# Kernel tuning notes

Hardware: AMD Instinct MI355X
Metric: run time of the kernel (lower is better)

## Reference

```python
import jax, jax.numpy as jnp
import numpy as np

N_NODES = 50000
N_EDGES = 800000
ND = 64   # node_dim
HD = 128  # hidden_dim
ED = 32   # edge_dim


def setup_inputs() -> dict:
    key = jax.random.key(0)
    ks = jax.random.split(key, 16)
    init = lambda k, shape: (jax.random.normal(k, shape, jnp.float32)
                             / np.float32(np.sqrt(shape[0])))
    h = jax.random.normal(ks[0], (N_NODES, ND), jnp.float32)
    x = jax.random.normal(ks[1], (N_NODES, 3), jnp.float32) * 10.0
    edge_index = jax.random.randint(ks[2], (2, N_EDGES), 0, N_NODES, dtype=jnp.int64)
    # realistic edge distances = actual pairwise distances of sampled edges
    edge_dist = jnp.linalg.norm(x[edge_index[0]] - x[edge_index[1]], axis=-1)
    in_dim = 2 * ND + ED
    return {
        "h": h, "x": x, "edge_index": edge_index, "edge_dist": edge_dist,
        # edge_mlp: Linear(1, ED) -> SiLU -> Linear(ED, ED)
        "We1": init(ks[3], (1, ED)), "be1": jnp.zeros((ED,), jnp.float32),
        "We2": init(ks[4], (ED, ED)), "be2": jnp.zeros((ED,), jnp.float32),
        # node_mlp: Linear(in_dim, HD) -> SiLU -> Linear(HD, ND)
        "Wn1": init(ks[5], (in_dim, HD)), "bn1": jnp.zeros((HD,), jnp.float32),
        "Wn2": init(ks[6], (HD, ND)), "bn2": jnp.zeros((ND,), jnp.float32),
        # coord_mlp: Linear(in_dim, HD) -> SiLU -> Linear(HD, 1, bias=False)
        "Wc1": init(ks[7], (in_dim, HD)), "bc1": jnp.zeros((HD,), jnp.float32),
        "Wc2": init(ks[8], (HD, 1)),
    }


def reference(h, x, edge_index, edge_dist,
              We1, be1, We2, be2,
              Wn1, bn1, Wn2, bn2,
              Wc1, bc1, Wc2):
    n = h.shape[0]
    src, dst = edge_index[0], edge_index[1]
    # edge_mlp on scalar distance -> [E, ED]
    e = jax.nn.silu(edge_dist[:, None] @ We1 + be1) @ We2 + be2
    # gather + concat -> [E, 2*ND + ED]
    m_input = jnp.concatenate([h[src], h[dst], e], axis=-1)
    # node messages [E, ND]
    m = jax.nn.silu(m_input @ Wn1 + bn1) @ Wn2 + bn2
    h_agg = jax.ops.segment_sum(m, dst, num_segments=n)
    # coord update weight [E, 1]
    coord_weight = jax.nn.silu(m_input @ Wc1 + bc1) @ Wc2
    dir_vec = x[src] - x[dst]
    dir_len = jnp.clip(jnp.linalg.norm(dir_vec, axis=-1, keepdims=True), 1e-8)
    coord_update = coord_weight * (dir_vec / dir_len)
    x_agg = jax.ops.segment_sum(coord_update, dst, num_segments=n)
    return h + h_agg, x + x_agg
```

## Files before the change

kernel.cpp:

```cpp
#include <hip/hip_runtime.h>


#define NN 50000
#define NE 800000
#define NDIM 64
#define HDIM 128
#define EDIM 32
#define NTILES (NE / 64)
#define MSTRIDE 168
#define HSTRIDE 136
#define NH (NN * NDIM)
#define NX (NN * 3)

typedef __bf16 bf16x8 __attribute__((ext_vector_type(8)));
typedef float f32x4 __attribute__((ext_vector_type(4)));
typedef unsigned short ushort8 __attribute__((ext_vector_type(8)));
typedef unsigned short ushort4v __attribute__((ext_vector_type(4)));

__device__ __forceinline__ unsigned short f2bf(float f) {
    union { float f; unsigned int u; } c; c.f = f;
    unsigned int r = c.u + 0x7fffu + ((c.u >> 16) & 1u);
    return (unsigned short)(r >> 16);
}
__device__ __forceinline__ float bf2f(unsigned short u) {
    union { unsigned int u; float f; } c; c.u = ((unsigned int)u) << 16;
    return c.f;
}
__device__ __forceinline__ float silu(float v) { return v / (1.0f + __expf(-v)); }

__device__ __forceinline__ bf16x8 ld_frag(const unsigned short* p) {
    union { ushort8 u; bf16x8 v; } c;
    c.u = *(const ushort8*)p;
    return c.v;
}
__device__ __forceinline__ bf16x8 mk_frag(const unsigned short* u) {
    union { ushort8 uu; bf16x8 v; } c;
#pragma unroll
    for (int j = 0; j < 8; ++j) c.uu[j] = u[j];
    return c.v;
}

__global__ void init_out(const float* __restrict__ h, const float* __restrict__ x,
                         float* __restrict__ out) {
    int i = blockIdx.x * 256 + threadIdx.x;
    if (i < NH) out[i] = h[i];
    else if (i < NH + NX) out[i] = x[i - NH];
}

__global__ __launch_bounds__(256, 2) void egnn_edges(
    const float* __restrict__ h, const float* __restrict__ x,
    const int* __restrict__ srcg, const int* __restrict__ dstg,
    const float* __restrict__ dist,
    const float* __restrict__ We1, const float* __restrict__ be1,
    const float* __restrict__ We2, const float* __restrict__ be2,
    const float* __restrict__ Wn1, const float* __restrict__ bn1,
    const float* __restrict__ Wn2, const float* __restrict__ bn2,
    const float* __restrict__ Wc1, const float* __restrict__ bc1,
    const float* __restrict__ Wc2,
    float* __restrict__ outh, float* __restrict__ outx) {

    __shared__ __align__(16) unsigned short mlds[64 * MSTRIDE];
    __shared__ __align__(16) unsigned short hl[64 * HSTRIDE];
    __shared__ int src_l[64];
    __shared__ int dst_l[64];
    __shared__ float dist_l[64];
    __shared__ float we1_l[32], be1_l[32], be2_l[32];
    __shared__ float we2_l[32 * 32];
    __shared__ float wc2_l[128];
    __shared__ float part_l[256];

    const int tid  = threadIdx.x;
    const int w    = tid >> 6;
    const int lane = tid & 63;
    const int l15  = lane & 15;
    const int quad = lane >> 4;

    if (tid < 32) { we1_l[tid] = We1[tid]; be1_l[tid] = be1[tid]; be2_l[tid] = be2[tid]; }
    if (tid < 128) wc2_l[tid] = Wc2[tid];
    for (int i = tid; i < 1024; i += 256) we2_l[i] = We2[i];

    bf16x8 wn1f[5][2], wc1f[5][2];
#pragma unroll
    for (int kc = 0; kc < 5; ++kc) {
#pragma unroll
        for (int nt = 0; nt < 2; ++nt) {
            unsigned short un[8], uc[8];
            const int n = w * 32 + nt * 16 + l15;
#pragma unroll
            for (int j = 0; j < 8; ++j) {
                const int k = kc * 32 + quad * 8 + j;
                un[j] = f2bf(Wn1[k * HDIM + n]);
                uc[j] = f2bf(Wc1[k * HDIM + n]);
            }
            wn1f[kc][nt] = mk_frag(un);
            wc1f[kc][nt] = mk_frag(uc);
        }
    }
    bf16x8 wn2f[4];
#pragma unroll
    for (int kc = 0; kc < 4; ++kc) {
        unsigned short u[8];
        const int n = w * 16 + l15;
#pragma unroll
        for (int j = 0; j < 8; ++j) {
            const int k = kc * 32 + quad * 8 + j;
            u[j] = f2bf(Wn2[k * NDIM + n]);
        }
        wn2f[kc] = mk_frag(u);
    }
    const float biasN0 = bn1[w * 32 + l15];
    const float biasN1 = bn1[w * 32 + 16 + l15];
    const float biasC0 = bc1[w * 32 + l15];
    const float biasC1 = bc1[w * 32 + 16 + l15];
    const float bias2v = bn2[w * 16 + l15];

    for (int tile = blockIdx.x; tile < NTILES; tile += gridDim.x) {
        __syncthreads();

        if (tid < 64) {
            const int e = tile * 64 + tid;
            src_l[tid] = srcg[e];
            dst_l[tid] = dstg[e];
            dist_l[tid] = dist[e];
        }
        __syncthreads();

        {
            const int c4 = tid & 15, sub = tid >> 4;
#pragma unroll
            for (int it = 0; it < 4; ++it) {
                const int el = sub + it * 16;
                const float4 hs = *(const float4*)(h + (size_t)src_l[el] * NDIM + c4 * 4);
                const float4 hd = *(const float4*)(h + (size_t)dst_l[el] * NDIM + c4 * 4);
                ushort4v us = { f2bf(hs.x), f2bf(hs.y), f2bf(hs.z), f2bf(hs.w) };
                ushort4v ud = { f2bf(hd.x), f2bf(hd.y), f2bf(hd.z), f2bf(hd.w) };
                *(ushort4v*)&mlds[el * MSTRIDE + c4 * 4] = us;
                *(ushort4v*)&mlds[el * MSTRIDE + 64 + c4 * 4] = ud;
            }
        }
        {
            const int el = tid >> 2, part = tid & 3;
            const float dv = dist_l[el];
            float o[8];
#pragma unroll
            for (int j = 0; j < 8; ++j) o[j] = be2_l[part * 8 + j];
#pragma unroll
            for (int k = 0; k < 32; ++k) {
                const float sk = silu(dv * we1_l[k] + be1_l[k]);
#pragma unroll
                for (int j = 0; j < 8; ++j) o[j] += sk * we2_l[k * 32 + part * 8 + j];
            }
            ushort4v a = { f2bf(o[0]), f2bf(o[1]), f2bf(o[2]), f2bf(o[3]) };
            ushort4v b = { f2bf(o[4]), f2bf(o[5]), f2bf(o[6]), f2bf(o[7]) };
            *(ushort4v*)&mlds[el * MSTRIDE + 128 + part * 8] = a;
            *(ushort4v*)&mlds[el * MSTRIDE + 128 + part * 8 + 4] = b;
        }
        __syncthreads();

        f32x4 accN[4][2], accC[4][2];
#pragma unroll
        for (int mt = 0; mt < 4; ++mt) {
            accN[mt][0] = (f32x4){biasN0, biasN0, biasN0, biasN0};
            accN[mt][1] = (f32x4){biasN1, biasN1, biasN1, biasN1};
            accC[mt][0] = (f32x4){biasC0, biasC0, biasC0, biasC0};
            accC[mt][1] = (f32x4){biasC1, biasC1, biasC1, biasC1};
        }
#pragma unroll
        for (int kc = 0; kc < 5; ++kc) {
            bf16x8 af[4];
#pragma unroll
            for (int mt = 0; mt < 4; ++mt)
                af[mt] = ld_frag(&mlds[(mt * 16 + l15) * MSTRIDE + kc * 32 + quad * 8]);
#pragma unroll
            for (int mt = 0; mt < 4; ++mt) {
#pragma unroll
                for (int nt = 0; nt < 2; ++nt) {
                    accN[mt][nt] = __builtin_amdgcn_mfma_f32_16x16x32_bf16(
                        af[mt], wn1f[kc][nt], accN[mt][nt], 0, 0, 0);
                    accC[mt][nt] = __builtin_amdgcn_mfma_f32_16x16x32_bf16(
                        af[mt], wc1f[kc][nt], accC[mt][nt], 0, 0, 0);
                }
            }
        }

#pragma unroll
        for (int mt = 0; mt < 4; ++mt)
#pragma unroll
            for (int nt = 0; nt < 2; ++nt)
#pragma unroll
                for (int r = 0; r < 4; ++r)
                    hl[(mt * 16 + quad * 4 + r) * HSTRIDE + w * 32 + nt * 16 + l15] =
                        f2bf(silu(accN[mt][nt][r]));
        __syncthreads();

        f32x4 acc2[4];
#pragma unroll
        for (int mt = 0; mt < 4; ++mt) acc2[mt] = (f32x4){bias2v, bias2v, bias2v, bias2v};
#pragma unroll
        for (int kc = 0; kc < 4; ++kc) {
#pragma unroll
            for (int mt = 0; mt < 4; ++mt) {
                bf16x8 a2 = ld_frag(&hl[(mt * 16 + l15) * HSTRIDE + kc * 32 + quad * 8]);
                acc2[mt] = __builtin_amdgcn_mfma_f32_16x16x32_bf16(a2, wn2f[kc], acc2[mt], 0, 0, 0);
            }
        }
#pragma unroll
        for (int mt = 0; mt < 4; ++mt) {
#pragma unroll
            for (int r = 0; r < 4; ++r) {
                const int el = mt * 16 + quad * 4 + r;
                atomicAdd(outh + (size_t)dst_l[el] * NDIM + w * 16 + l15, acc2[mt][r]);
            }
        }
        __syncthreads();

#pragma unroll
        for (int mt = 0; mt < 4; ++mt)
#pragma unroll
            for (int nt = 0; nt < 2; ++nt)
#pragma unroll
                for (int r = 0; r < 4; ++r)
                    hl[(mt * 16 + quad * 4 + r) * HSTRIDE + w * 32 + nt * 16 + l15] =
                        f2bf(silu(accC[mt][nt][r]));
        __syncthreads();

        {
            const int el = tid & 63, part = tid >> 6;
            float s = 0.0f;
#pragma unroll
            for (int k = 0; k < 32; ++k) {
                const int kk = part * 32 + k;
                s += bf2f(hl[el * HSTRIDE + kk]) * wc2_l[kk];
            }
            part_l[part * 64 + el] = s;
        }
        __syncthreads();

        if (tid < 64) {
            const float cw = part_l[tid] + part_l[64 + tid] + part_l[128 + tid] + part_l[192 + tid];
            const int sn = src_l[tid], dn = dst_l[tid];
            const float dx = x[sn * 3 + 0] - x[dn * 3 + 0];
            const float dy = x[sn * 3 + 1] - x[dn * 3 + 1];
            const float dz = x[sn * 3 + 2] - x[dn * 3 + 2];
            float len = sqrtf(dx * dx + dy * dy + dz * dz);
            len = fmaxf(len, 1e-8f);
            const float f = cw / len;
            atomicAdd(outx + (size_t)dn * 3 + 0, f * dx);
            atomicAdd(outx + (size_t)dn * 3 + 1, f * dy);
            atomicAdd(outx + (size_t)dn * 3 + 2, f * dz);
        }
    }
}

extern "C" void kernel_launch(void* const* d_in, const int* in_sizes, int n_in,
                              void* d_out, int out_size, void* d_ws, size_t ws_size,
                              hipStream_t stream) {
    const float* h    = (const float*)d_in[0];
    const float* x    = (const float*)d_in[1];
    const int*   ei   = (const int*)d_in[2];
    const float* dist = (const float*)d_in[3];
    const float* We1  = (const float*)d_in[4];
    const float* be1  = (const float*)d_in[5];
    const float* We2  = (const float*)d_in[6];
    const float* be2  = (const float*)d_in[7];
    const float* Wn1  = (const float*)d_in[8];
    const float* bn1  = (const float*)d_in[9];
    const float* Wn2  = (const float*)d_in[10];
    const float* bn2  = (const float*)d_in[11];
    const float* Wc1  = (const float*)d_in[12];
    const float* bc1  = (const float*)d_in[13];
    const float* Wc2  = (const float*)d_in[14];

    float* outh = (float*)d_out;
    float* outx = outh + (size_t)NH;

    init_out<<<(NH + NX + 255) / 256, 256, 0, stream>>>(h, x, (float*)d_out);
    egnn_edges<<<512, 256, 0, stream>>>(h, x, ei, ei + NE, dist,
                                        We1, be1, We2, be2,
                                        Wn1, bn1, Wn2, bn2,
                                        Wc1, bc1, Wc2,
                                        outh, outx);
}
```

Measured before the change: 418.4 us.

## Fold edge MLP second layer into first GEMM, prepack bf16 h, fuse coord reduction

Precomputes We2·Wn1/Wc1 (and bias folding) in a prep kernel so the per-edge edge-MLP only needs SiLU of the first layer, removing the 32x32 per-edge matmul. Converts h to bf16 once so gathers read half the bytes, permutes hidden columns so SiLU results store as packed pairs, and replaces the LDS round-trip for the coord weight with an in-register shuffle reduction. Raises occupancy target to 3 blocks/SM and doubles grid size. Adds extra prep launches and workspace use, and folding weights in bf16 changes rounding slightly.

```diff
diff --git a/kernel.cpp b/kernel.cpp
--- a/kernel.cpp
+++ b/kernel.cpp
@@ -5,13 +5,18 @@
 #define NE 800000
 #define NDIM 64
 #define HDIM 128
-#define EDIM 32
 #define NTILES (NE / 64)
 #define MSTRIDE 168
 #define HSTRIDE 136
 #define NH (NN * NDIM)
 #define NX (NN * 3)
 
+#define WS_HBF    0
+#define WS_WN1P   6400000
+#define WS_WC1P   6440960
+#define WS_BN1P   6481920
+#define WS_BC1P   6482432
+
 typedef __bf16 bf16x8 __attribute__((ext_vector_type(8)));
 typedef float f32x4 __attribute__((ext_vector_type(4)));
 typedef unsigned short ushort8 __attribute__((ext_vector_type(8)));
@@ -22,12 +27,12 @@
     unsigned int r = c.u + 0x7fffu + ((c.u >> 16) & 1u);
     return (unsigned short)(r >> 16);
 }
-__device__ __forceinline__ float bf2f(unsigned short u) {
-    union { unsigned int u; float f; } c; c.u = ((unsigned int)u) << 16;
-    return c.f;
-}
-__device__ __forceinline__ float silu(float v) { return v / (1.0f + __expf(-v)); }
-
+__device__ __forceinline__ unsigned int pk2bf(float a, float b) {
+    return (unsigned int)f2bf(a) | ((unsigned int)f2bf(b) << 16);
+}
+__device__ __forceinline__ float silu(float v) {
+    return v * __builtin_amdgcn_rcpf(1.0f + __expf(-v));
+}
 __device__ __forceinline__ bf16x8 ld_frag(const unsigned short* p) {
     union { ushort8 u; bf16x8 v; } c;
     c.u = *(const ushort8*)p;
@@ -47,15 +52,58 @@
     else if (i < NH + NX) out[i] = x[i - NH];
 }
 
-__global__ __launch_bounds__(256, 2) void egnn_edges(
-    const float* __restrict__ h, const float* __restrict__ x,
+__global__ void prep_h(const float* __restrict__ h, unsigned short* __restrict__ hbf) {
+    int i = (blockIdx.x * 256 + threadIdx.x) * 4;
+    if (i < NH) {
+        float4 v = *(const float4*)(h + i);
+        ushort4v u = { f2bf(v.x), f2bf(v.y), f2bf(v.z), f2bf(v.w) };
+        *(ushort4v*)(hbf + i) = u;
+    }
+}
+
+__global__ void prep_w(const float* __restrict__ We2, const float* __restrict__ be2,
+                       const float* __restrict__ Wn1, const float* __restrict__ bn1,
+                       const float* __restrict__ Wc1, const float* __restrict__ bc1,
+                       unsigned short* __restrict__ wn1p, unsigned short* __restrict__ wc1p,
+                       float* __restrict__ bn1p, float* __restrict__ bc1p) {
+    int idx = blockIdx.x * 256 + threadIdx.x;
+    if (idx >= 160 * 128) return;
+    int k = idx >> 7, n = idx & 127;
+    float vn, vc;
+    if (k < 128) {
+        vn = Wn1[k * HDIM + n];
+        vc = Wc1[k * HDIM + n];
+    } else {
+        int i = k - 128;
+        float sn = 0.0f, sc = 0.0f;
+        for (int j = 0; j < 32; ++j) {
+            float w = We2[i * 32 + j];
+            sn += w * Wn1[(128 + j) * HDIM + n];
+            sc += w * Wc1[(128 + j) * HDIM + n];
+        }
+        vn = sn; vc = sc;
+    }
+    wn1p[idx] = f2bf(vn);
+    wc1p[idx] = f2bf(vc);
+    if (idx < 128) {
+        float sn = bn1[idx], sc = bc1[idx];
+        for (int j = 0; j < 32; ++j) {
+            sn += be2[j] * Wn1[(128 + j) * HDIM + idx];
+            sc += be2[j] * Wc1[(128 + j) * HDIM + idx];
+        }
+        bn1p[idx] = sn;
+        bc1p[idx] = sc;
+    }
+}
+
+__global__ __launch_bounds__(256, 3) void egnn_edges(
+    const unsigned short* __restrict__ hbf, const float* __restrict__ x,
     const int* __restrict__ srcg, const int* __restrict__ dstg,
     const float* __restrict__ dist,
     const float* __restrict__ We1, const float* __restrict__ be1,
-    const float* __restrict__ We2, const float* __restrict__ be2,
-    const float* __restrict__ Wn1, const float* __restrict__ bn1,
+    const unsigned short* __restrict__ wn1p, const float* __restrict__ bn1p,
     const float* __restrict__ Wn2, const float* __restrict__ bn2,
-    const float* __restrict__ Wc1, const float* __restrict__ bc1,
+    const unsigned short* __restrict__ wc1p, const float* __restrict__ bc1p,
     const float* __restrict__ Wc2,
     float* __restrict__ outh, float* __restrict__ outx) {
 
@@ -64,9 +112,6 @@
     __shared__ int src_l[64];
     __shared__ int dst_l[64];
     __shared__ float dist_l[64];
-    __shared__ float we1_l[32], be1_l[32], be2_l[32];
-    __shared__ float we2_l[32 * 32];
-    __shared__ float wc2_l[128];
     __shared__ float part_l[256];
 
     const int tid  = threadIdx.x;
@@ -75,22 +120,18 @@
     const int l15  = lane & 15;
     const int quad = lane >> 4;
 
-    if (tid < 32) { we1_l[tid] = We1[tid]; be1_l[tid] = be1[tid]; be2_l[tid] = be2[tid]; }
-    if (tid < 128) wc2_l[tid] = Wc2[tid];
-    for (int i = tid; i < 1024; i += 256) we2_l[i] = We2[i];
-
     bf16x8 wn1f[5][2], wc1f[5][2];
 #pragma unroll
     for (int kc = 0; kc < 5; ++kc) {
 #pragma unroll
         for (int nt = 0; nt < 2; ++nt) {
             unsigned short un[8], uc[8];
-            const int n = w * 32 + nt * 16 + l15;
+            const int n = w * 32 + l15 * 2 + nt;
 #pragma unroll
             for (int j = 0; j < 8; ++j) {
                 const int k = kc * 32 + quad * 8 + j;
-                un[j] = f2bf(Wn1[k * HDIM + n]);
-                uc[j] = f2bf(Wc1[k * HDIM + n]);
+                un[j] = wn1p[k * HDIM + n];
+                uc[j] = wc1p[k * HDIM + n];
             }
             wn1f[kc][nt] = mk_frag(un);
             wc1f[kc][nt] = mk_frag(uc);
@@ -108,11 +149,13 @@
         }
         wn2f[kc] = mk_frag(u);
     }
-    const float biasN0 = bn1[w * 32 + l15];
-    const float biasN1 = bn1[w * 32 + 16 + l15];
-    const float biasC0 = bc1[w * 32 + l15];
-    const float biasC1 = bc1[w * 32 + 16 + l15];
+    const float biasN0 = bn1p[w * 32 + l15 * 2];
+    const float biasN1 = bn1p[w * 32 + l15 * 2 + 1];
+    const float biasC0 = bc1p[w * 32 + l15 * 2];
+    const float biasC1 = bc1p[w * 32 + l15 * 2 + 1];
     const float bias2v = bn2[w * 16 + l15];
+    const float wc2a = Wc2[w * 32 + l15 * 2];
+    const float wc2b = Wc2[w * 32 + l15 * 2 + 1];
 
     for (int tile = blockIdx.x; tile < NTILES; tile += gridDim.x) {
         __syncthreads();
@@ -126,34 +169,25 @@
         __syncthreads();
 
         {
-            const int c4 = tid & 15, sub = tid >> 4;
-#pragma unroll
-            for (int it = 0; it < 4; ++it) {
-                const int el = sub + it * 16;
-                const float4 hs = *(const float4*)(h + (size_t)src_l[el] * NDIM + c4 * 4);
-                const float4 hd = *(const float4*)(h + (size_t)dst_l[el] * NDIM + c4 * 4);
-                ushort4v us = { f2bf(hs.x), f2bf(hs.y), f2bf(hs.z), f2bf(hs.w) };
-                ushort4v ud = { f2bf(hd.x), f2bf(hd.y), f2bf(hd.z), f2bf(hd.w) };
-                *(ushort4v*)&mlds[el * MSTRIDE + c4 * 4] = us;
-                *(ushort4v*)&mlds[el * MSTRIDE + 64 + c4 * 4] = ud;
+            const int c8 = tid & 7, sub = tid >> 3;
+#pragma unroll
+            for (int it = 0; it < 2; ++it) {
+                const int el = sub + it * 32;
+                const ushort8 hs = *(const ushort8*)(hbf + (size_t)src_l[el] * NDIM + c8 * 8);
+                const ushort8 hd = *(const ushort8*)(hbf + (size_t)dst_l[el] * NDIM + c8 * 8);
+                *(ushort8*)&mlds[el * MSTRIDE + c8 * 8] = hs;
+                *(ushort8*)&mlds[el * MSTRIDE + 64 + c8 * 8] = hd;
             }
         }
         {
-            const int el = tid >> 2, part = tid & 3;
-            const float dv = dist_l[el];
-            float o[8];
-#pragma unroll
-            for (int j = 0; j < 8; ++j) o[j] = be2_l[part * 8 + j];
-#pragma unroll
-            for (int k = 0; k < 32; ++k) {
-                const float sk = silu(dv * we1_l[k] + be1_l[k]);
-#pragma unroll
-                for (int j = 0; j < 8; ++j) o[j] += sk * we2_l[k * 32 + part * 8 + j];
-            }
-            ushort4v a = { f2bf(o[0]), f2bf(o[1]), f2bf(o[2]), f2bf(o[3]) };
-            ushort4v b = { f2bf(o[4]), f2bf(o[5]), f2bf(o[6]), f2bf(o[7]) };
-            *(ushort4v*)&mlds[el * MSTRIDE + 128 + part * 8] = a;
-            *(ushort4v*)&mlds[el * MSTRIDE + 128 + part * 8 + 4] = b;
+            const float dv = dist_l[lane];
+            ushort8 su;
+#pragma unroll
+            for (int j = 0; j < 8; ++j) {
+                const int k = w * 8 + j;
+                su[j] = f2bf(silu(fmaf(dv, We1[k], be1[k])));
+            }
+            *(ushort8*)&mlds[lane * MSTRIDE + 128 + w * 8] = su;
         }
         __syncthreads();
 
@@ -184,13 +218,14 @@
         }
 
 #pragma unroll
-        for (int mt = 0; mt < 4; ++mt)
-#pragma unroll
-            for (int nt = 0; nt < 2; ++nt)
-#pragma unroll
-                for (int r = 0; r < 4; ++r)
-                    hl[(mt * 16 + quad * 4 + r) * HSTRIDE + w * 32 + nt * 16 + l15] =
-                        f2bf(silu(accN[mt][nt][r]));
+        for (int mt = 0; mt < 4; ++mt) {
+#pragma unroll
+            for (int r = 0; r < 4; ++r) {
+                const int row = mt * 16 + quad * 4 + r;
+                *(unsigned int*)&hl[row * HSTRIDE + w * 32 + l15 * 2] =
+                    pk2bf(silu(accN[mt][0][r]), silu(accN[mt][1][r]));
+            }
+        }
         __syncthreads();
 
         f32x4 acc2[4];
@@ -212,27 +247,29 @@
                 atomicAdd(outh + (size_t)dst_l[el] * NDIM + w * 16 + l15, acc2[mt][r]);
             }
         }
-        __syncthreads();
-
-#pragma unroll
-        for (int mt = 0; mt < 4; ++mt)
-#pragma unroll
-            for (int nt = 0; nt < 2; ++nt)
+
+        {
+            float vals[16];
+#pragma unroll
+            for (int mt = 0; mt < 4; ++mt)
 #pragma unroll
                 for (int r = 0; r < 4; ++r)
-                    hl[(mt * 16 + quad * 4 + r) * HSTRIDE + w * 32 + nt * 16 + l15] =
-                        f2bf(silu(accC[mt][nt][r]));
-        __syncthreads();
-
-        {
-            const int el = tid & 63, part = tid >> 6;
-            float s = 0.0f;
-#pragma unroll
-            for (int k = 0; k < 32; ++k) {
-                const int kk = part * 32 + k;
-                s += bf2f(hl[el * HSTRIDE + kk]) * wc2_l[kk];
-            }
-            part_l[part * 64 + el] = s;
+                    vals[mt * 4 + r] = silu(accC[mt][0][r]) * wc2a +
+                                       silu(accC[mt][1][r]) * wc2b;
+#pragma unroll
+            for (int m = 8; m >= 1; m >>= 1) {
+                const bool up = (l15 & m) != 0;
+#pragma unroll
+                for (int j = 0; j < 8; ++j) {
+                    if (j < m) {
+                        float send = up ? vals[j] : vals[j + m];
+                        float recv = __shfl_xor(send, m, 64);
+                        vals[j] = (up ? vals[j + m] : vals[j]) + recv;
+                    }
+                }
+            }
+            const int edge = ((l15 >> 2) << 4) + (quad << 2) + (l15 & 3);
+            part_l[w * 64 + edge] = vals[0];
         }
         __syncthreads();
 
@@ -271,13 +308,21 @@
     const float* bc1  = (const float*)d_in[13];
     const float* Wc2  = (const float*)d_in[14];
 
+    unsigned short* hbf  = (unsigned short*)((char*)d_ws + WS_HBF);
+    unsigned short* wn1p = (unsigned short*)((char*)d_ws + WS_WN1P);
+    unsigned short* wc1p = (unsigned short*)((char*)d_ws + WS_WC1P);
+    float* bn1p = (float*)((char*)d_ws + WS_BN1P);
+    float* bc1p = (float*)((char*)d_ws + WS_BC1P);
+
     float* outh = (float*)d_out;
     float* outx = outh + (size_t)NH;
 
+    prep_h<<<(NH / 4 + 255) / 256, 256, 0, stream>>>(h, hbf);
+    prep_w<<<(160 * 128 + 255) / 256, 256, 0, stream>>>(We2, be2, Wn1, bn1, Wc1, bc1,
+                                                        wn1p, wc1p, bn1p, bc1p);
     init_out<<<(NH + NX + 255) / 256, 256, 0, stream>>>(h, x, (float*)d_out);
-    egnn_edges<<<512, 256, 0, stream>>>(h, x, ei, ei + NE, dist,
-                                        We1, be1, We2, be2,
-                                        Wn1, bn1, Wn2, bn2,
-                                        Wc1, bc1, Wc2,
-                                        outh, outx);
-}
+    egnn_edges<<<1024, 256, 0, stream>>>(hbf, x, ei, ei + NE, dist,
+                                         We1, be1, wn1p, bn1p,
+                                         Wn2, bn2, wc1p, bc1p, Wc2,
+                                         outh, outx);
+}
```

After: 598.3 us. 43.0% more time.
